# Performance work log

Measured on AMD Instinct MI355X. Metric: run time of the kernel, lower is better.

The kernel has to match this reference:

```python
import jax, jax.numpy as jnp
import numpy as np

B, N, R, S, H, D, HIDDEN = 4, 1028, 4, 32, 12, 64, 32
L = (2 * S - 1) ** 2  # 3969 relative-position bins


def _build_tables():
    # CPB relative-coordinate table (signed log1p-normalized offsets)
    rng = np.arange(-(S - 1), S, dtype=np.float32)
    dY, dX = np.meshgrid(rng, rng, indexing='ij')
    rel = np.stack([dY / max(S - 1, 1), dX / max(S - 1, 1)], -1).reshape(-1, 2)
    rel_table = np.sign(rel) * np.log1p(np.abs(rel))  # [L, 2]
    # 2D relative-position index table over the SxS patch grid
    Y, X = np.meshgrid(np.arange(S), np.arange(S), indexing='ij')
    flat = np.stack([Y, X], 0).reshape(2, -1)          # [2, P]
    d = flat[:, :, None] - flat[:, None, :]            # [2, P, P]
    d = np.transpose(d, (1, 2, 0)).copy()              # [P, P, 2]
    d[:, :, 0] += S - 1
    d[:, :, 1] += S - 1
    d[:, :, 0] *= 2 * S - 1
    l_idx = d.sum(-1)                                  # [P, P] in [0, L)
    idx = np.full((N, N), -1, dtype=np.int64)          # -1 sentinel for register tokens
    idx[R:, R:] = l_idx
    return jnp.asarray(rel_table, jnp.float32), jnp.asarray(idx)


def setup_inputs() -> dict:
    key = jax.random.key(0)
    ks = jax.random.split(key, 8)
    rel_table, idx_table = _build_tables()
    return {
        'q': jax.random.normal(ks[0], (B, H, N, D), jnp.float32),
        'k': jax.random.normal(ks[1], (B, H, N, D), jnp.float32),
        'v': jax.random.normal(ks[2], (B, H, N, D), jnp.float32),
        'mu': jax.random.normal(ks[3], (B, 2 * H, N), jnp.float32),
        'rel_table': rel_table,                              # [L, 2] buffer
        'W1': jax.random.normal(ks[4], (HIDDEN, 2), jnp.float32) * 0.5,
        'b1': jax.random.normal(ks[5], (HIDDEN,), jnp.float32) * 0.1,
        'W2': jax.random.normal(ks[6], (H, HIDDEN), jnp.float32) * 0.05,
        'gamma': jax.random.normal(ks[7], (H,), jnp.float32),
        'idx_table': idx_table,                              # [N, N] int64
    }


def reference(q, k, v, mu, rel_table, W1, b1, W2, gamma, idx_table):
    # CPB MLP: Linear(2->hidden) + exact GELU + Linear(hidden->H, no bias)
    hid = jax.nn.gelu(rel_table @ W1.T + b1, approximate=False)   # [L, HIDDEN]
    bt = hid @ W2.T                                               # [L, H]
    bt_ext = jnp.concatenate([jnp.zeros((1, H), bt.dtype), bt], 0)  # [L+1, H]
    bias = bt_ext[idx_table + 1]                                  # [N, N, H]; sentinel -1 -> zero row

    # per-token gates: signed log1p transform then q-side + k-side split
    mu_t = jnp.sign(mu) * jnp.log1p(jnp.abs(mu))                  # [B, 2H, N]
    mu_q, mu_k = mu_t[:, :H], mu_t[:, H:]                         # each [B, H, N]
    g = mu_q[:, :, :, None] + mu_k[:, :, None, :]                 # [B, H, N, N]
    gam = jax.nn.sigmoid(gamma)[None, :, None, None]              # [1, H, 1, 1]

    scale = 1.0 / jnp.sqrt(jnp.asarray(D, jnp.float32))
    scores = jnp.einsum('bhqd,bhkd->bhqk', q, k) * scale
    scores = scores + gam * g * jnp.transpose(bias, (2, 0, 1))[None]  # [B, H, N, N]
    attn = jax.nn.softmax(scores, axis=-1)
    return jnp.einsum('bhqk,bhkd->bhqd', attn, v)
```

## Files before the change

### kernel.cpp

```cpp
#include <hip/hip_runtime.h>

#define B_ 4
#define H_ 12
#define N_ 1028
#define D_ 64
#define R_ 4
#define L_ 3969
#define HID_ 32
#define KBLK 64
#define NT_ 17
#define NBH_ 48
#define QBLK 128
#define NQT 9
#define NWG (NBH_*NQT)
#define TBL 3973
#define MUKP 1088
#define LOG2E 1.4426950408889634f
#define SCL1 (0.125f*LOG2E)
#define THR_ 8.0f

typedef __attribute__((ext_vector_type(8)))  short bf16x8;
typedef __attribute__((ext_vector_type(4)))  float f32x4;
typedef __attribute__((ext_vector_type(2)))  unsigned int u32x2;
typedef __attribute__((ext_vector_type(4)))  unsigned int u32x4;
typedef __attribute__((address_space(3))) unsigned int lds_u32;
typedef const __attribute__((address_space(1))) unsigned int glb_u32;

__device__ __forceinline__ unsigned pkbf(float lo, float hi) {
  unsigned r;
  asm("v_cvt_pk_bf16_f32 %0, %1, %2" : "=v"(r) : "v"(lo), "v"(hi));
  return r;
}
__device__ __forceinline__ float exp2_fast(float x) {
  float r; asm("v_exp_f32 %0, %1" : "=v"(r) : "v"(x)); return r;
}
__device__ __forceinline__ float sgnlog1p(float x) {
  float t = log1pf(fabsf(x));
  return (x > 0.f) ? t : ((x < 0.f) ? -t : 0.f);
}

__global__ __launch_bounds__(256) void prep_kernel(
    const float* __restrict__ rel, const float* __restrict__ W1,
    const float* __restrict__ b1, const float* __restrict__ W2,
    const float* __restrict__ gammag, const float* __restrict__ kg,
    const float* __restrict__ vg, const float* __restrict__ mug,
    float* __restrict__ btgf, float* __restrict__ mut,
    unsigned short* __restrict__ kv)
{
  const int blk = blockIdx.x, tid = threadIdx.x;
  if (blk < 16) {
    if (blk == 0 && tid < 48) btgf[(tid >> 2)*TBL + (tid & 3)] = 0.f;
    int l = blk*256 + tid;
    if (l < L_) {
      float r0 = rel[2*l], r1 = rel[2*l+1];
      float hid[HID_];
#pragma unroll
      for (int j = 0; j < HID_; ++j) {
        float x = W1[2*j]*r0 + W1[2*j+1]*r1 + b1[j];
        hid[j] = 0.5f * x * (1.f + erff(x * 0.70710678118654752f));
      }
#pragma unroll
      for (int h = 0; h < H_; ++h) {
        float acc = 0.f;
#pragma unroll
        for (int j = 0; j < HID_; ++j) acc += W2[h*HID_+j]*hid[j];
        float gscl = LOG2E / (1.f + __expf(-gammag[h]));
        btgf[h*TBL + 4 + l] = gscl * acc;
      }
    }
  } else if (blk < 16 + NBH_*NT_) {
    const int idx = blk - 16;
    const int bh = idx / NT_, t = idx - bh*NT_;
    const int k0 = t * KBLK;
    const float* kb = kg + (size_t)bh*N_*D_;
    const float* vb = vg + (size_t)bh*N_*D_;
    unsigned short* Ko = kv + (size_t)idx*8192;
    unsigned short* Vo = Ko + 4096;
    const int kcb = tid >> 4, d4 = (tid & 15)*4;
#pragma unroll
    for (int i = 0; i < 4; ++i) {
      int kc = kcb + i*16;
      int kr = k0 + kc; if (kr >= N_) kr = N_-1;
      f32x4 a = *(const f32x4*)(kb + (size_t)kr*D_ + d4);
      *(u32x2*)&Ko[kc*64 + (d4 ^ ((kc & 7) << 3))] = (u32x2){pkbf(a[0],a[1]), pkbf(a[2],a[3])};
    }
    const int vd0 = (tid >> 4)*4, vkc0 = (tid & 15)*4;
    const int loc = vkc0 & 31;
    const int p0 = 32*(vkc0 >> 5) + 8*((loc >> 2) & 3) + 4*(loc >> 4);
    f32x4 r[4];
#pragma unroll
    for (int i = 0; i < 4; ++i) {
      int kr = k0 + vkc0 + i; if (kr >= N_) kr = N_-1;
      r[i] = *(const f32x4*)(vb + (size_t)kr*D_ + vd0);
    }
#pragma unroll
    for (int j = 0; j < 4; ++j) {
      int d = vd0 + j;
      int addr = d*64 + ((p0 & 56) ^ ((d & 7) << 3)) + (p0 & 7);
      *(u32x2*)&Vo[addr] = (u32x2){pkbf(r[0][j],r[1][j]), pkbf(r[2][j],r[3][j])};
    }
  } else {
    int idx = (blk - (16 + NBH_*NT_))*256 + tid;
    if (idx < NBH_*N_) {
      int bh = idx / N_, n = idx - bh*N_;
      int b = bh / H_, h = bh - b*H_;
      mut[idx] = sgnlog1p(mug[((size_t)b*2*H_ + H_ + h)*N_ + n]);
    }
  }
}

__global__ __launch_bounds__(512, 4) void attn_kernel(
    const float* __restrict__ qg, const float* __restrict__ mug,
    const float* __restrict__ btgf, const float* __restrict__ mut,
    const unsigned short* __restrict__ kv, float* __restrict__ outg)
{
  __shared__ __align__(16) unsigned short KV[2][8192];
  __shared__ __align__(16) float btgs[TBL];
  __shared__ __align__(16) float muks[MUKP];

  const int tid = threadIdx.x;
  const int w = tid >> 6, lane = tid & 63, g = lane >> 4, c = lane & 15;

  const int orig = blockIdx.x;
  const int wg = (orig & 7)*(NWG/8) + (orig >> 3);
  const int bh = wg / NQT;
  const int qt = wg - bh*NQT;
  const int b = bh / H_, h = bh - b*H_;
  const int q0 = qt * QBLK;

  const float* qb = qg + (size_t)bh*N_*D_;
  const unsigned short* kvb = kv + (size_t)bh*NT_*8192;

  {
    const float* bth = btgf + h*TBL;
    for (int i = tid; i < TBL; i += 512) btgs[i] = bth[i];
    const float* mt = mut + (size_t)bh*N_;
    for (int i = tid; i < MUKP; i += 512) muks[i] = mt[i < N_ ? i : N_-1];
  }

  const int qrow = q0 + 16*w + c;
  const int qrc = qrow < N_ ? qrow : N_-1;
  bf16x8 qf[2];
#pragma unroll
  for (int ch = 0; ch < 2; ++ch) {
    const float* p = qb + (size_t)qrc*D_ + ch*32 + 8*g;
    f32x4 a0 = *(const f32x4*)p;
    f32x4 a1 = *(const f32x4*)(p + 4);
    u32x4 qw;
    qw[0] = pkbf(a0[0]*SCL1, a0[1]*SCL1); qw[1] = pkbf(a0[2]*SCL1, a0[3]*SCL1);
    qw[2] = pkbf(a1[0]*SCL1, a1[1]*SCL1); qw[3] = pkbf(a1[2]*SCL1, a1[3]*SCL1);
    qf[ch] = __builtin_bit_cast(bf16x8, qw);
  }
  const float muq_c = (qrow < N_) ? sgnlog1p(mug[((size_t)b*2*H_ + h)*N_ + qrow]) : 0.f;
  const int qi = qrow - R_;
  const bool qok = (qi >= 0) && (qrow < N_);
  const int qy = qi >> 5, qx = qi & 31;
  const int lqc = qy*63 + qx + 1988;

  int va[4];
#pragma unroll
  for (int kt = 0; kt < 4; ++kt) {
    int ki0 = kt*16 + 4*g - R_;
    int lk  = (ki0 >> 5)*63 + (ki0 & 31);
    va[kt]  = lqc - lk;
  }

  auto issue = [&](int tt, int pp) {
    const char* src = (const char*)(kvb + (size_t)tt*8192) + w*2048;
    char* dst = (char*)&KV[pp][0] + w*2048;
#pragma unroll
    for (int j = 0; j < 2; ++j) {
      int o = j*1024;
      __builtin_amdgcn_global_load_lds((glb_u32*)(src + o + lane*16),
                                       (lds_u32*)(dst + o), 16, 0, 0);
    }
  };

  float mrun = -3.0e38f, lrun = 0.f;
  f32x4 O[4];
#pragma unroll
  for (int dt = 0; dt < 4; ++dt) O[dt] = (f32x4){0.f,0.f,0.f,0.f};

  issue(0, 0);

  for (int t = 0; t < NT_; ++t) {
    const int k0 = t * KBLK;
    const int p = t & 1;

    asm volatile("s_waitcnt vmcnt(0)" ::: "memory");
    __syncthreads();
    if (t + 1 < NT_) issue(t + 1, p ^ 1);

    const unsigned short* Kl = &KV[p][0];
    const unsigned short* Vl = &KV[p][4096];

    f32x4 sc[4];
    __builtin_amdgcn_s_setprio(1);
#pragma unroll
    for (int kt = 0; kt < 4; ++kt) {
      int row = kt*16 + c;
      int sw = (row & 7) << 3;
      bf16x8 ka0 = *(const bf16x8*)&Kl[row*64 + ((8*g) ^ sw)];
      bf16x8 ka1 = *(const bf16x8*)&Kl[row*64 + ((32 + 8*g) ^ sw)];
      f32x4 s = (f32x4){0.f,0.f,0.f,0.f};
      s = __builtin_amdgcn_mfma_f32_16x16x32_bf16(ka0, qf[0], s, 0, 0, 0);
      s = __builtin_amdgcn_mfma_f32_16x16x32_bf16(ka1, qf[1], s, 0, 0, 0);
      sc[kt] = s;
    }
    __builtin_amdgcn_s_setprio(0);

    float smax = -3.0e38f;
    if (t == 0) {
#pragma unroll
      for (int kt = 0; kt < 4; ++kt) {
        const f32x4 mk = *(const f32x4*)&muks[kt*16 + 4*g];
        bool okq = qok && (kt > 0 || g > 0);
        int basep = okq ? va[kt] : 3;
        f32x4 bv;
        bv[0] = btgs[basep-3]; bv[1] = btgs[basep-2];
        bv[2] = btgs[basep-1]; bv[3] = btgs[basep];
        f32x4 s = sc[kt];
#pragma unroll
        for (int r = 0; r < 4; ++r) {
          float val = s[r] + (muq_c + mk[r]) * bv[3-r];
          s[r] = val;
          smax = fmaxf(smax, val);
        }
        sc[kt] = s;
      }
    } else if (t < NT_-1) {
#pragma unroll
      for (int kt = 0; kt < 4; ++kt) {
        const f32x4 mk = *(const f32x4*)&muks[k0 + kt*16 + 4*g];
        int basep = qok ? va[kt] : 3;
        f32x4 bv;
        bv[0] = btgs[basep-3]; bv[1] = btgs[basep-2];
        bv[2] = btgs[basep-1]; bv[3] = btgs[basep];
        f32x4 s = sc[kt];
#pragma unroll
        for (int r = 0; r < 4; ++r) {
          float val = s[r] + (muq_c + mk[r]) * bv[3-r];
          s[r] = val;
          smax = fmaxf(smax, val);
        }
        sc[kt] = s;
      }
    } else {
#pragma unroll
      for (int kt = 0; kt < 4; ++kt) {
        const f32x4 mk = *(const f32x4*)&muks[k0 + kt*16 + 4*g];
        int ki0 = k0 + kt*16 + 4*g - R_;
        bool mq = (ki0 < 1024);
        bool okq = mq && qok;
        int basep = okq ? va[kt] : 3;
        f32x4 bv;
        bv[0] = btgs[basep-3]; bv[1] = btgs[basep-2];
        bv[2] = btgs[basep-1]; bv[3] = btgs[basep];
        f32x4 s = sc[kt];
#pragma unroll
        for (int r = 0; r < 4; ++r) {
          float val = s[r] + (muq_c + mk[r]) * bv[3-r];
          val = mq ? val : -3.0e38f;
          s[r] = val;
          smax = fmaxf(smax, val);
        }
        sc[kt] = s;
      }
    }
#pragma unroll
    for (int kt = 0; kt < 4; ++kt) va[kt] -= 126;
    smax = fmaxf(smax, __shfl_xor(smax, 16));
    smax = fmaxf(smax, __shfl_xor(smax, 32));

    if (__any(smax > mrun + THR_)) {
      float mnew = fmaxf(mrun, smax);
      float corr = exp2_fast(mrun - mnew);
      lrun *= corr;
#pragma unroll
      for (int dt = 0; dt < 4; ++dt)
#pragma unroll
        for (int r = 0; r < 4; ++r) O[dt][r] *= corr;
      mrun = mnew;
    }

    float psum = 0.f;
#pragma unroll
    for (int kt = 0; kt < 4; ++kt)
#pragma unroll
      for (int r = 0; r < 4; ++r) {
        float pv = exp2_fast(sc[kt][r] - mrun);
        sc[kt][r] = pv;
        psum += pv;
      }
    lrun += psum;

    u32x4 pa[2];
#pragma unroll
    for (int kh = 0; kh < 2; ++kh) {
      pa[kh][0] = pkbf(sc[2*kh][0],   sc[2*kh][1]);
      pa[kh][1] = pkbf(sc[2*kh][2],   sc[2*kh][3]);
      pa[kh][2] = pkbf(sc[2*kh+1][0], sc[2*kh+1][1]);
      pa[kh][3] = pkbf(sc[2*kh+1][2], sc[2*kh+1][3]);
    }

    __builtin_amdgcn_s_setprio(1);
#pragma unroll
    for (int kh = 0; kh < 2; ++kh) {
      bf16x8 pfr = __builtin_bit_cast(bf16x8, pa[kh]);
      int sw = (c & 7) << 3;
#pragma unroll
      for (int dt = 0; dt < 4; ++dt) {
        int d = dt*16 + c;
        bf16x8 va2 = *(const bf16x8*)&Vl[d*64 + ((32*kh + 8*g) ^ sw)];
        O[dt] = __builtin_amdgcn_mfma_f32_16x16x32_bf16(va2, pfr, O[dt], 0, 0, 0);
      }
    }
    __builtin_amdgcn_s_setprio(0);
  }

  lrun += __shfl_xor(lrun, 16);
  lrun += __shfl_xor(lrun, 32);
  float rlv = 1.f / lrun;
  const int qo = q0 + 16*w + c;
  if (qo < N_) {
    float* ob = outg + ((size_t)bh*N_ + qo)*64;
#pragma unroll
    for (int dt = 0; dt < 4; ++dt) {
      f32x4 ov;
#pragma unroll
      for (int r = 0; r < 4; ++r) ov[r] = O[dt][r] * rlv;
      *(f32x4*)(ob + dt*16 + 4*g) = ov;
    }
  }
}

extern "C" void kernel_launch(void* const* d_in, const int* in_sizes, int n_in,
                              void* d_out, int out_size, void* d_ws, size_t ws_size,
                              hipStream_t stream) {
  const float* q     = (const float*)d_in[0];
  const float* k     = (const float*)d_in[1];
  const float* v     = (const float*)d_in[2];
  const float* mu    = (const float*)d_in[3];
  const float* rel   = (const float*)d_in[4];
  const float* W1    = (const float*)d_in[5];
  const float* b1    = (const float*)d_in[6];
  const float* W2    = (const float*)d_in[7];
  const float* gamma = (const float*)d_in[8];

  char* wsb = (char*)d_ws;
  float* btgf = (float*)wsb;
  float* mut  = (float*)(wsb + 190704);
  unsigned short* kvimg = (unsigned short*)(wsb + 388080);

  const int prep_blocks = 16 + NBH_*NT_ + (NBH_*N_ + 255)/256;
  prep_kernel<<<dim3(prep_blocks), dim3(256), 0, stream>>>(rel, W1, b1, W2, gamma,
                                                           k, v, mu, btgf, mut, kvimg);
  attn_kernel<<<dim3(NWG), dim3(512), 0, stream>>>(q, mu, btgf, mut, kvimg,
                                                   (float*)d_out);
}
```

Baseline: 56.36 us.

## Software-pipeline QK^T one tile ahead with triple-buffered K/V in LDS

Moves the QK^T MFMA for tile t+1 ahead of the softmax and PV work for tile t, and triple-buffers the K/V LDS tiles so prefetch of tile t+2 can overlap. The aim is to let the matrix units run while the VALU does bias, exp and packing, hiding latency inside each iteration. In exchange it raises LDS use by another 16 KB per block and adds a second set of score registers, which may lower occupancy under the 512-thread, 4-block launch bound.

```diff
diff --git a/kernel.cpp b/kernel.cpp
--- a/kernel.cpp
+++ b/kernel.cpp
@@ -114,7 +114,7 @@
     const float* __restrict__ btgf, const float* __restrict__ mut,
     const unsigned short* __restrict__ kv, float* __restrict__ outg)
 {
-  __shared__ __align__(16) unsigned short KV[2][8192];
+  __shared__ __align__(16) unsigned short KV[3][8192];
   __shared__ __align__(16) float btgs[TBL];
   __shared__ __align__(16) float muks[MUKP];
 
@@ -175,26 +175,8 @@
                                        (lds_u32*)(dst + o), 16, 0, 0);
     }
   };
-
-  float mrun = -3.0e38f, lrun = 0.f;
-  f32x4 O[4];
-#pragma unroll
-  for (int dt = 0; dt < 4; ++dt) O[dt] = (f32x4){0.f,0.f,0.f,0.f};
-
-  issue(0, 0);
-
-  for (int t = 0; t < NT_; ++t) {
-    const int k0 = t * KBLK;
-    const int p = t & 1;
-
-    asm volatile("s_waitcnt vmcnt(0)" ::: "memory");
-    __syncthreads();
-    if (t + 1 < NT_) issue(t + 1, p ^ 1);
-
-    const unsigned short* Kl = &KV[p][0];
-    const unsigned short* Vl = &KV[p][4096];
-
-    f32x4 sc[4];
+  auto STcompute = [&](int bp, f32x4* out) {
+    const unsigned short* Kl = &KV[bp][0];
     __builtin_amdgcn_s_setprio(1);
 #pragma unroll
     for (int kt = 0; kt < 4; ++kt) {
@@ -205,9 +187,37 @@
       f32x4 s = (f32x4){0.f,0.f,0.f,0.f};
       s = __builtin_amdgcn_mfma_f32_16x16x32_bf16(ka0, qf[0], s, 0, 0, 0);
       s = __builtin_amdgcn_mfma_f32_16x16x32_bf16(ka1, qf[1], s, 0, 0, 0);
-      sc[kt] = s;
+      out[kt] = s;
     }
     __builtin_amdgcn_s_setprio(0);
+  };
+
+  float mrun = -3.0e38f, lrun = 0.f;
+  f32x4 O[4];
+#pragma unroll
+  for (int dt = 0; dt < 4; ++dt) O[dt] = (f32x4){0.f,0.f,0.f,0.f};
+
+  f32x4 scA[4], scB[4];
+
+  issue(0, 0);
+  asm volatile("s_waitcnt vmcnt(0)" ::: "memory");
+  __syncthreads();
+  issue(1, 1);
+  STcompute(0, scA);
+
+  int bufPV = 0;
+
+  for (int t = 0; t < NT_; ++t) {
+    const int k0 = t * KBLK;
+    int bufS = bufPV + 1; if (bufS >= 3) bufS = 0;
+    int bufStage = bufS + 1; if (bufStage >= 3) bufStage = 0;
+
+    if (t + 1 < NT_) {
+      asm volatile("s_waitcnt vmcnt(0)" ::: "memory");
+      __syncthreads();
+      if (t + 2 < NT_) issue(t + 2, bufStage);
+      STcompute(bufS, scB);
+    }
 
     float smax = -3.0e38f;
     if (t == 0) {
@@ -219,14 +229,12 @@
         f32x4 bv;
         bv[0] = btgs[basep-3]; bv[1] = btgs[basep-2];
         bv[2] = btgs[basep-1]; bv[3] = btgs[basep];
-        f32x4 s = sc[kt];
 #pragma unroll
         for (int r = 0; r < 4; ++r) {
-          float val = s[r] + (muq_c + mk[r]) * bv[3-r];
-          s[r] = val;
+          float val = scA[kt][r] + (muq_c + mk[r]) * bv[3-r];
+          scA[kt][r] = val;
           smax = fmaxf(smax, val);
         }
-        sc[kt] = s;
       }
     } else if (t < NT_-1) {
 #pragma unroll
@@ -236,14 +244,12 @@
         f32x4 bv;
         bv[0] = btgs[basep-3]; bv[1] = btgs[basep-2];
         bv[2] = btgs[basep-1]; bv[3] = btgs[basep];
-        f32x4 s = sc[kt];
 #pragma unroll
         for (int r = 0; r < 4; ++r) {
-          float val = s[r] + (muq_c + mk[r]) * bv[3-r];
-          s[r] = val;
+          float val = scA[kt][r] + (muq_c + mk[r]) * bv[3-r];
+          scA[kt][r] = val;
           smax = fmaxf(smax, val);
         }
-        sc[kt] = s;
       }
     } else {
 #pragma unroll
@@ -256,15 +262,13 @@
         f32x4 bv;
         bv[0] = btgs[basep-3]; bv[1] = btgs[basep-2];
         bv[2] = btgs[basep-1]; bv[3] = btgs[basep];
-        f32x4 s = sc[kt];
 #pragma unroll
         for (int r = 0; r < 4; ++r) {
-          float val = s[r] + (muq_c + mk[r]) * bv[3-r];
+          float val = scA[kt][r] + (muq_c + mk[r]) * bv[3-r];
           val = mq ? val : -3.0e38f;
-          s[r] = val;
+          scA[kt][r] = val;
           smax = fmaxf(smax, val);
         }
-        sc[kt] = s;
       }
     }
 #pragma unroll
@@ -288,8 +292,8 @@
     for (int kt = 0; kt < 4; ++kt)
 #pragma unroll
       for (int r = 0; r < 4; ++r) {
-        float pv = exp2_fast(sc[kt][r] - mrun);
-        sc[kt][r] = pv;
+        float pv = exp2_fast(scA[kt][r] - mrun);
+        scA[kt][r] = pv;
         psum += pv;
       }
     lrun += psum;
@@ -297,25 +301,34 @@
     u32x4 pa[2];
 #pragma unroll
     for (int kh = 0; kh < 2; ++kh) {
-      pa[kh][0] = pkbf(sc[2*kh][0],   sc[2*kh][1]);
-      pa[kh][1] = pkbf(sc[2*kh][2],   sc[2*kh][3]);
-      pa[kh][2] = pkbf(sc[2*kh+1][0], sc[2*kh+1][1]);
-      pa[kh][3] = pkbf(sc[2*kh+1][2], sc[2*kh+1][3]);
-    }
-
-    __builtin_amdgcn_s_setprio(1);
-#pragma unroll
-    for (int kh = 0; kh < 2; ++kh) {
-      bf16x8 pfr = __builtin_bit_cast(bf16x8, pa[kh]);
-      int sw = (c & 7) << 3;
-#pragma unroll
-      for (int dt = 0; dt < 4; ++dt) {
-        int d = dt*16 + c;
-        bf16x8 va2 = *(const bf16x8*)&Vl[d*64 + ((32*kh + 8*g) ^ sw)];
-        O[dt] = __builtin_amdgcn_mfma_f32_16x16x32_bf16(va2, pfr, O[dt], 0, 0, 0);
-      }
-    }
-    __builtin_amdgcn_s_setprio(0);
+      pa[kh][0] = pkbf(scA[2*kh][0],   scA[2*kh][1]);
+      pa[kh][1] = pkbf(scA[2*kh][2],   scA[2*kh][3]);
+      pa[kh][2] = pkbf(scA[2*kh+1][0], scA[2*kh+1][1]);
+      pa[kh][3] = pkbf(scA[2*kh+1][2], scA[2*kh+1][3]);
+    }
+
+    {
+      const unsigned short* Vl = &KV[bufPV][4096];
+      __builtin_amdgcn_s_setprio(1);
+#pragma unroll
+      for (int kh = 0; kh < 2; ++kh) {
+        bf16x8 pfr = __builtin_bit_cast(bf16x8, pa[kh]);
+        int sw = (c & 7) << 3;
+#pragma unroll
+        for (int dt = 0; dt < 4; ++dt) {
+          int d = dt*16 + c;
+          bf16x8 va2 = *(const bf16x8*)&Vl[d*64 + ((32*kh + 8*g) ^ sw)];
+          O[dt] = __builtin_amdgcn_mfma_f32_16x16x32_bf16(va2, pfr, O[dt], 0, 0, 0);
+        }
+      }
+      __builtin_amdgcn_s_setprio(0);
+    }
+
+    if (t + 1 < NT_) {
+#pragma unroll
+      for (int kt = 0; kt < 4; ++kt) scA[kt] = scB[kt];
+    }
+    bufPV = bufS;
   }
 
   lrun += __shfl_xor(lrun, 16);
```

Result: slower. 58.50 us (+3.8%).
